# Kernel tuning notes

Measured on AMD Instinct MI355X. Metric: run time of the kernel, lower is better.

Reference implementation:

```python
import jax, jax.numpy as jnp
import numpy as np

C_IN, H, W = 8, 32, 32
C_OUT, K, S, P = 32, 4, 2, 1
HO = (H + 2 * P - K) // S + 1  # 16
WO = (W + 2 * P - K) // S + 1  # 16
IN_FEAT = C_IN * H * W          # 8192
OUT_FEAT = C_OUT * HO * WO      # 8192


def conv2d(x, w, b=None):
    # x: [N, C_in, H, W], w: [C_out, C_in, K, K]
    y = jax.lax.conv_general_dilated(
        x, w, window_strides=(S, S), padding=[(P, P), (P, P)],
        dimension_numbers=("NCHW", "OIHW", "NCHW"))
    if b is not None:
        y = y + b[None, :, None, None]
    return y


def toeplitz_matrix(weight):
    # Equivalent to torch.autograd.functional.jacobian of flatten(conv(x)):
    # conv is linear, so apply it to the identity basis (batched conv).
    eye = jnp.eye(IN_FEAT, dtype=weight.dtype).reshape(IN_FEAT, C_IN, H, W)
    cols = conv2d(eye, weight).reshape(IN_FEAT, OUT_FEAT)  # column j = conv(e_j)
    return cols.T  # [OUT_FEAT, IN_FEAT]


def setup_inputs() -> dict:
    key = jax.random.key(0)
    k1, k2, k3, k4 = jax.random.split(key, 4)
    center = jax.random.normal(k1, (C_IN, H, W), jnp.float32)
    eps = 0.01 * jax.random.uniform(k2, (C_IN, H, W), jnp.float32)
    bounds = jnp.stack([center - eps, center + eps], 0)  # [2, C_in, H, W]
    weight = 0.1 * jax.random.normal(k3, (C_OUT, C_IN, K, K), jnp.float32)
    bias = 0.1 * jax.random.normal(k4, (C_OUT,), jnp.float32)
    assignment = jnp.zeros((C_OUT, HO, WO), jnp.int32)  # unused by forward
    return {"bounds": bounds, "weight": weight, "bias": bias,
            "assignment": assignment}


def reference(bounds, weight, bias, assignment):
    W_plus = jnp.maximum(weight, 0.0)
    W_minus = jnp.minimum(weight, 0.0)
    half_b = bias / 2.0
    l = bounds[0][None]  # [1, C_in, H, W]
    u = bounds[1][None]
    # upper = conv_plus(u) + conv_minus(l); each conv carries bias/2
    upper = conv2d(u, W_plus, half_b) + conv2d(l, W_minus, half_b)
    lower = conv2d(l, W_plus, half_b) + conv2d(u, W_minus, half_b)
    out_bounds = jnp.concatenate([lower, upper], 0)  # [2, C_out, HO, WO]

    # back-substitution (terminal branch: predecessor is the input layer)
    W_mat = toeplitz_matrix(weight)                 # [OUT_FEAT, IN_FEAT]
    bias_backsub = jnp.repeat(bias, HO * WO)        # repeat_interleave
    Mp = jnp.maximum(W_mat, 0.0)
    Mm = jnp.minimum(W_mat, 0.0)
    lf = bounds[0].reshape(-1)
    uf = bounds[1].reshape(-1)
    new_l = (Mp @ lf + Mm @ uf + bias_backsub).reshape(C_OUT, HO, WO)
    new_u = (Mp @ uf + Mm @ lf + bias_backsub).reshape(C_OUT, HO, WO)
    # tighten: keep the better of forward-propagated and back-substituted
    out_bounds = out_bounds.at[0].set(jnp.where(new_l > out_bounds[0], new_l, out_bounds[0]))
    out_bounds = out_bounds.at[1].set(jnp.where(new_u < out_bounds[1], new_u, out_bounds[1]))
    return out_bounds, W_mat, bias_backsub
```

## Files before the change

kernel.cpp:

```cpp
#include <hip/hip_runtime.h>

#define C_IN   8
#define HH     32
#define WW     32
#define C_OUT  32
#define KK     4
#define SS     2
#define PP     1
#define HO     16
#define WO     16
#define IN_FEAT  8192
#define OUT_FEAT 8192

__global__ __launch_bounds__(256) void zero_wmat(float4* __restrict__ wmat) {
    const int stride = 16384 * 256;
    int idx = blockIdx.x * 256 + threadIdx.x;
#pragma unroll
    for (int it = 0; it < 4; ++it, idx += stride)
        wmat[idx] = make_float4(0.f, 0.f, 0.f, 0.f);
}

__global__ __launch_bounds__(256) void scatter_bounds(const float* __restrict__ bounds,
                                                      const float* __restrict__ weight,
                                                      const float* __restrict__ bias,
                                                      float* __restrict__ wmat,
                                                      float* __restrict__ out_bounds,
                                                      float* __restrict__ bias_bs) {
    const int row  = (blockIdx.x * 256 + threadIdx.x) >> 6;
    const int lane = threadIdx.x & 63;

    const int c_out = row >> 8;
    const int ho    = (row >> 4) & 15;
    const int wo    = row & 15;

    const float* lptr = bounds;
    const float* uptr = bounds + IN_FEAT;

    float lo = 0.f, up = 0.f;
#pragma unroll
    for (int s = 0; s < 2; ++s) {
        const int t  = lane + 64 * s;
        const int ci = t >> 4;
        const int kh = (t >> 2) & 3;
        const int kw = t & 3;
        const int h  = ho * SS - PP + kh;
        const int w  = wo * SS - PP + kw;
        if ((unsigned)h < (unsigned)HH && (unsigned)w < (unsigned)WW) {
            const float wv  = weight[(c_out * C_IN + ci) * (KK * KK) + kh * KK + kw];
            const int   col = ci * (HH * WW) + h * WW + w;
            wmat[(size_t)row * IN_FEAT + col] = wv;
            const float lv = lptr[col];
            const float uv = uptr[col];
            const float wp = fmaxf(wv, 0.f);
            const float wm = fminf(wv, 0.f);
            lo = fmaf(wp, lv, fmaf(wm, uv, lo));
            up = fmaf(wp, uv, fmaf(wm, lv, up));
        }
    }
#pragma unroll
    for (int off = 32; off; off >>= 1) {
        lo += __shfl_down(lo, off, 64);
        up += __shfl_down(up, off, 64);
    }
    if (lane == 0) {
        const float b = bias[c_out];
        out_bounds[row]            = lo + b;
        out_bounds[OUT_FEAT + row] = up + b;
        bias_bs[row] = b;
    }
}

extern "C" void kernel_launch(void* const* d_in, const int* in_sizes, int n_in,
                              void* d_out, int out_size, void* d_ws, size_t ws_size,
                              hipStream_t stream) {
    const float* bounds = (const float*)d_in[0];
    const float* weight = (const float*)d_in[1];
    const float* bias   = (const float*)d_in[2];

    float* out     = (float*)d_out;
    float* wmat    = out + 2 * OUT_FEAT;
    float* bias_bs = out + 2 * OUT_FEAT + (size_t)OUT_FEAT * IN_FEAT;

    zero_wmat<<<16384, 256, 0, stream>>>((float4*)wmat);
    scatter_bounds<<<2048, 256, 0, stream>>>(bounds, weight, bias, wmat, out, bias_bs);
}
```

Measured before the change: 264.9 us.

## Fuse zero-fill and scatter into one row-wise Toeplitz writer kernel

Replaces the separate zero-fill kernel and the sparse scatter kernel with one kernel where each wavefront writes a full Toeplitz row as float4 stores. Nonzero weights are inserted inline and the bounds accumulation happens in the same pass. This removes a second launch and the scattered read-modify traffic on the 256MB matrix, so the output is written exactly once. The cost is per-element branch logic inside the store loop.

```diff
diff --git a/kernel.cpp b/kernel.cpp
--- a/kernel.cpp
+++ b/kernel.cpp
@@ -12,51 +12,63 @@
 #define IN_FEAT  8192
 #define OUT_FEAT 8192
 
-__global__ __launch_bounds__(256) void zero_wmat(float4* __restrict__ wmat) {
-    const int stride = 16384 * 256;
-    int idx = blockIdx.x * 256 + threadIdx.x;
-#pragma unroll
-    for (int it = 0; it < 4; ++it, idx += stride)
-        wmat[idx] = make_float4(0.f, 0.f, 0.f, 0.f);
-}
-
-__global__ __launch_bounds__(256) void scatter_bounds(const float* __restrict__ bounds,
-                                                      const float* __restrict__ weight,
-                                                      const float* __restrict__ bias,
-                                                      float* __restrict__ wmat,
-                                                      float* __restrict__ out_bounds,
-                                                      float* __restrict__ bias_bs) {
-    const int row  = (blockIdx.x * 256 + threadIdx.x) >> 6;
+__global__ __launch_bounds__(256) void fused_row_kernel(const float* __restrict__ bounds,
+                                                        const float* __restrict__ weight,
+                                                        const float* __restrict__ bias,
+                                                        float* __restrict__ wmat,
+                                                        float* __restrict__ out_bounds,
+                                                        float* __restrict__ bias_bs) {
+    const int gid  = blockIdx.x * 256 + threadIdx.x;
+    const int row  = gid >> 6;
     const int lane = threadIdx.x & 63;
 
     const int c_out = row >> 8;
     const int ho    = (row >> 4) & 15;
     const int wo    = row & 15;
+    const int hs    = ho * SS - PP;
+    const int ws    = wo * SS - PP;
 
     const float* lptr = bounds;
     const float* uptr = bounds + IN_FEAT;
+    float* __restrict__ rout = wmat + (size_t)row * IN_FEAT;
 
     float lo = 0.f, up = 0.f;
+
+#pragma unroll 8
+    for (int it = 0; it < 32; ++it) {
+        const int col0 = it * 256 + lane * 4;
+        const int ci   = col0 >> 10;
+        const int h    = (col0 >> 5) & 31;
+        const int w0   = col0 & 31;
+
+        const int kh  = h  - hs;
+        const int kwb = w0 - ws;
+
+        float4 v = make_float4(0.f, 0.f, 0.f, 0.f);
+        if ((unsigned)kh < (unsigned)KK && kwb >= -3 && kwb <= 3) {
+            const float4 wr = *reinterpret_cast<const float4*>(
+                weight + ((c_out * C_IN + ci) * (KK * KK) + kh * KK));
+            float* vp = &v.x;
 #pragma unroll
-    for (int s = 0; s < 2; ++s) {
-        const int t  = lane + 64 * s;
-        const int ci = t >> 4;
-        const int kh = (t >> 2) & 3;
-        const int kw = t & 3;
-        const int h  = ho * SS - PP + kh;
-        const int w  = wo * SS - PP + kw;
-        if ((unsigned)h < (unsigned)HH && (unsigned)w < (unsigned)WW) {
-            const float wv  = weight[(c_out * C_IN + ci) * (KK * KK) + kh * KK + kw];
-            const int   col = ci * (HH * WW) + h * WW + w;
-            wmat[(size_t)row * IN_FEAT + col] = wv;
-            const float lv = lptr[col];
-            const float uv = uptr[col];
-            const float wp = fmaxf(wv, 0.f);
-            const float wm = fminf(wv, 0.f);
-            lo = fmaf(wp, lv, fmaf(wm, uv, lo));
-            up = fmaf(wp, uv, fmaf(wm, lv, up));
+            for (int j = 0; j < 4; ++j) {
+                const int kw = kwb + j;
+                if ((unsigned)kw < (unsigned)KK) {
+                    const float wv = (kw == 0) ? wr.x : (kw == 1) ? wr.y
+                                   : (kw == 2) ? wr.z : wr.w;
+                    vp[j] = wv;
+                    const int col = col0 + j;
+                    const float lv = lptr[col];
+                    const float uv = uptr[col];
+                    const float wp = fmaxf(wv, 0.f);
+                    const float wm = fminf(wv, 0.f);
+                    lo = fmaf(wp, lv, fmaf(wm, uv, lo));
+                    up = fmaf(wp, uv, fmaf(wm, lv, up));
+                }
+            }
         }
+        *reinterpret_cast<float4*>(rout + col0) = v;
     }
+
 #pragma unroll
     for (int off = 32; off; off >>= 1) {
         lo += __shfl_down(lo, off, 64);
@@ -81,6 +93,5 @@
     float* wmat    = out + 2 * OUT_FEAT;
     float* bias_bs = out + 2 * OUT_FEAT + (size_t)OUT_FEAT * IN_FEAT;
 
-    zero_wmat<<<16384, 256, 0, stream>>>((float4*)wmat);
-    scatter_bounds<<<2048, 256, 0, stream>>>(bounds, weight, bias, wmat, out, bias_bs);
+    fused_row_kernel<<<2048, 256, 0, stream>>>(bounds, weight, bias, wmat, out, bias_bs);
 }
```

Result: no change. 262.9 us (-0.7%).

## Fuse zero-fill and weight scatter into a single row-wise Toeplitz writer

Applied to the files above, without the earlier changes.

Replaces the separate zero-fill kernel and scattered weight writes with one kernel where each wavefront writes its full Toeplitz row once as float4 stores, inserting weights in-register. Removes a second pass over the matrix and uncoalesced scatter stores. Uses fewer blocks with longer per-wave loops, which may lower memory-level parallelism.

```diff
diff --git a/kernel.cpp b/kernel.cpp
--- a/kernel.cpp
+++ b/kernel.cpp
@@ -12,30 +12,65 @@
 #define IN_FEAT  8192
 #define OUT_FEAT 8192
 
-__global__ __launch_bounds__(256) void zero_wmat(float4* __restrict__ wmat) {
-    const int stride = 16384 * 256;
-    int idx = blockIdx.x * 256 + threadIdx.x;
-#pragma unroll
-    for (int it = 0; it < 4; ++it, idx += stride)
-        wmat[idx] = make_float4(0.f, 0.f, 0.f, 0.f);
-}
-
-__global__ __launch_bounds__(256) void scatter_bounds(const float* __restrict__ bounds,
-                                                      const float* __restrict__ weight,
-                                                      const float* __restrict__ bias,
-                                                      float* __restrict__ wmat,
-                                                      float* __restrict__ out_bounds,
-                                                      float* __restrict__ bias_bs) {
-    const int row  = (blockIdx.x * 256 + threadIdx.x) >> 6;
+__global__ __launch_bounds__(256) void fused_row_kernel(const float* __restrict__ bounds,
+                                                        const float* __restrict__ weight,
+                                                        const float* __restrict__ bias,
+                                                        float* __restrict__ wmat,
+                                                        float* __restrict__ out_bounds,
+                                                        float* __restrict__ bias_bs) {
+    const int gid  = blockIdx.x * 256 + threadIdx.x;
+    const int row  = gid >> 6;
     const int lane = threadIdx.x & 63;
 
     const int c_out = row >> 8;
     const int ho    = (row >> 4) & 15;
     const int wo    = row & 15;
+    const int hs    = ho * SS - PP;
+    const int ws    = wo * SS - PP;
+
+    const int  lh   = lane >> 3;
+    const int  w0   = (lane & 7) * 4;
+    const int  kwb  = w0 - ws;
+    const bool whit = (kwb >= -3) & (kwb <= 3);
+
+    unsigned hbmask = 0;
+    {
+        const int loh = hs > 0 ? hs : 0;
+        const int hih = (hs + 3) < 31 ? (hs + 3) : 31;
+#pragma unroll
+        for (int hb = 0; hb < 4; ++hb)
+            if (hb * 8 <= hih && loh <= hb * 8 + 7) hbmask |= 1u << hb;
+    }
+    hbmask = __builtin_amdgcn_readfirstlane(hbmask);
+
+    const float4 zero4 = make_float4(0.f, 0.f, 0.f, 0.f);
+    float4* __restrict__ rp = reinterpret_cast<float4*>(wmat + (size_t)row * IN_FEAT) + lane;
+    const float* __restrict__ wco = weight + c_out * (C_IN * KK * KK);
+
+    for (int ci = 0; ci < C_IN; ++ci) {
+#pragma unroll
+        for (int hb = 0; hb < 4; ++hb, rp += 64) {
+            if (hbmask & (1u << hb)) {
+                float4 v = zero4;
+                const int kh = hb * 8 + lh - hs;
+                if (((unsigned)kh < (unsigned)KK) & whit) {
+                    const float* wb = wco + ci * (KK * KK) + kh * KK;
+                    float* vp = &v.x;
+#pragma unroll
+                    for (int j = 0; j < 4; ++j) {
+                        const int kw = kwb + j;
+                        if ((unsigned)kw < (unsigned)KK) vp[j] = wb[kw];
+                    }
+                }
+                *rp = v;
+            } else {
+                *rp = zero4;
+            }
+        }
+    }
 
     const float* lptr = bounds;
     const float* uptr = bounds + IN_FEAT;
-
     float lo = 0.f, up = 0.f;
 #pragma unroll
     for (int s = 0; s < 2; ++s) {
@@ -43,12 +78,11 @@
         const int ci = t >> 4;
         const int kh = (t >> 2) & 3;
         const int kw = t & 3;
-        const int h  = ho * SS - PP + kh;
-        const int w  = wo * SS - PP + kw;
+        const int h  = hs + kh;
+        const int w  = ws + kw;
         if ((unsigned)h < (unsigned)HH && (unsigned)w < (unsigned)WW) {
-            const float wv  = weight[(c_out * C_IN + ci) * (KK * KK) + kh * KK + kw];
+            const float wv  = wco[ci * (KK * KK) + kh * KK + kw];
             const int   col = ci * (HH * WW) + h * WW + w;
-            wmat[(size_t)row * IN_FEAT + col] = wv;
             const float lv = lptr[col];
             const float uv = uptr[col];
             const float wp = fmaxf(wv, 0.f);
@@ -81,6 +115,5 @@
     float* wmat    = out + 2 * OUT_FEAT;
     float* bias_bs = out + 2 * OUT_FEAT + (size_t)OUT_FEAT * IN_FEAT;
 
-    zero_wmat<<<16384, 256, 0, stream>>>((float4*)wmat);
-    scatter_bounds<<<2048, 256, 0, stream>>>(bounds, weight, bias, wmat, out, bias_bs);
+    fused_row_kernel<<<2048, 256, 0, stream>>>(bounds, weight, bias, wmat, out, bias_bs);
 }
```

Measured after the change: 259.7 us. Within noise of the previous version (-1.9%).
